# Optimization experiments

Hardware: AMD Instinct MI355X
Metric: run time of the kernel (lower is better)

## Reference

```python
import jax, jax.numpy as jnp
import numpy as np

DIM = 4096
HEADS = 32
HEAD_DIM = 128
FFN_INNER = 4 * DIM  # GEGLU inner
EPS = 1e-6


def _mk(key, shape, scale=0.02):
    return jax.random.normal(key, shape, dtype=jnp.float32) * scale


def setup_inputs() -> dict:
    key = jax.random.key(0)
    ks = jax.random.split(key, 20)
    inp = {
        "video": jax.random.normal(ks[0], (1, 4096, DIM), dtype=jnp.float32),
        "text": jax.random.normal(ks[1], (1, 256, DIM), dtype=jnp.float32),
        # self-attention projections
        "wq": _mk(ks[2], (DIM, DIM)),
        "wk": _mk(ks[3], (DIM, DIM)),
        "wv": _mk(ks[4], (DIM, DIM)),
        "wo": _mk(ks[5], (DIM, DIM)),
        "q_norm_w": jnp.ones((DIM,), jnp.float32),
        "k_norm_w": jnp.ones((DIM,), jnp.float32),
        # cross-attention projections (q from video, k/v from text)
        "cwq": _mk(ks[6], (DIM, DIM)),
        "cwk": _mk(ks[7], (DIM, DIM)),
        "cwv": _mk(ks[8], (DIM, DIM)),
        "cwo": _mk(ks[9], (DIM, DIM)),
        "cq_norm_w": jnp.ones((DIM,), jnp.float32),
        "ck_norm_w": jnp.ones((DIM,), jnp.float32),
        # GEGLU FFN: proj -> (value, gate) -> value * gelu(gate) -> down
        "w_ff_proj": _mk(ks[10], (DIM, 2 * FFN_INNER)),
        "w_ff_down": _mk(ks[11], (FFN_INNER, DIM)),
    }
    return inp


def rmsnorm(x, w, eps=EPS):
    # RMSNorm over full hidden dim in fp32 (matches DistributedRMSNorm global math)
    x32 = x.astype(jnp.float32)
    rms = jax.lax.rsqrt(jnp.mean(x32 * x32, axis=-1, keepdims=True) + eps)
    return (x32 * rms) * w


def split_heads(x):  # [b,s,dim] -> [b,h,s,hd]
    b, s, _ = x.shape
    return x.reshape(b, s, HEADS, HEAD_DIM).transpose(0, 2, 1, 3)


def merge_heads(x):  # [b,h,s,hd] -> [b,s,dim]
    b, h, s, hd = x.shape
    return x.transpose(0, 2, 1, 3).reshape(b, s, h * hd)


def bmm_sdpa(q, k, v):
    # BMM + softmax fallback (explicit score matrix, as on Neuron)
    scale = 1.0 / np.sqrt(HEAD_DIM)
    scores = jnp.einsum("bhqd,bhkd->bhqk", q, k) * scale
    probs = jax.nn.softmax(scores, axis=-1)
    return jnp.einsum("bhqk,bhkd->bhqd", probs, v)


def attention(x_q, x_kv, wq, wk, wv, wo, qn, kn):
    q = rmsnorm(x_q @ wq, qn)
    k = rmsnorm(x_kv @ wk, kn)
    v = x_kv @ wv
    out = bmm_sdpa(split_heads(q), split_heads(k), split_heads(v))
    return merge_heads(out) @ wo


def geglu_ffn(x, w_proj, w_down):
    h = x @ w_proj
    val, gate = jnp.split(h, 2, axis=-1)
    return (val * jax.nn.gelu(gate)) @ w_down


def reference(video, text, wq, wk, wv, wo, q_norm_w, k_norm_w,
              cwq, cwk, cwv, cwo, cq_norm_w, ck_norm_w,
              w_ff_proj, w_ff_down):
    # video self-attention block slice
    h = video + attention(video, video, wq, wk, wv, wo, q_norm_w, k_norm_w)
    # text cross-attention
    h = h + attention(h, text, cwq, cwk, cwv, cwo, cq_norm_w, ck_norm_w)
    # GEGLU feed-forward
    h = h + geglu_ffn(h, w_ff_proj, w_ff_down)
    return h
```

## Files before the change

### kernel.cpp

```cpp
#include <hip/hip_runtime.h>
#include <cstdint>
#include <cstddef>

typedef __bf16 bf16;
typedef __bf16 bf16x8 __attribute__((ext_vector_type(8)));
typedef __bf16 bf16x4 __attribute__((ext_vector_type(4)));
typedef float f32x4 __attribute__((ext_vector_type(4)));

static constexpr int D = 4096;
static constexpr int S = 4096;
static constexpr int T = 256;
static constexpr int H = 32;
static constexpr int F = 16384;

__device__ __forceinline__ void gload16(const void* g, void* l) {
  __builtin_amdgcn_global_load_lds((const __attribute__((address_space(1))) void*)g,
                                   (__attribute__((address_space(3))) void*)l, 16, 0, 0);
}

#define MFMA16(a, b, c) __builtin_amdgcn_mfma_f32_16x16x32_bf16((a), (b), (c), 0, 0, 0)

__global__ __launch_bounds__(256) void k_cvt(const float* __restrict__ in, bf16* __restrict__ out, int n) {
  int i = (blockIdx.x * 256 + threadIdx.x) * 4;
  if (i >= n) return;
  float4 v = *(const float4*)(in + i);
  bf16x4 o = { (bf16)v.x, (bf16)v.y, (bf16)v.z, (bf16)v.w };
  *(bf16x4*)(out + i) = o;
}

__global__ __launch_bounds__(256) void k_tc(const float* __restrict__ in, bf16* __restrict__ out,
                                            int R, int C, int ldin) {
  __shared__ float tile[64][65];
  const int c0 = blockIdx.x * 64, r0 = blockIdx.y * 64;
  const int x = threadIdx.x, y = threadIdx.y;
  #pragma unroll
  for (int i = 0; i < 16; i++) {
    const int yy = y + 4 * i;
    tile[yy][x] = in[(size_t)(r0 + yy) * ldin + c0 + x];
  }
  __syncthreads();
  #pragma unroll
  for (int i = 0; i < 16; i++) {
    const int yy = y + 4 * i;
    out[(size_t)(c0 + yy) * R + r0 + x] = (bf16)tile[x][yy];
  }
}

__global__ __launch_bounds__(256) void k_tb(const bf16* __restrict__ in, bf16* __restrict__ out, int R, int C) {
  __shared__ bf16 tile[32][33];
  int c0 = blockIdx.x * 32, r0 = blockIdx.y * 32;
  int x = threadIdx.x, y = threadIdx.y;
  #pragma unroll
  for (int yy = y; yy < 32; yy += 8)
    tile[yy][x] = in[(size_t)(r0 + yy) * C + c0 + x];
  __syncthreads();
  #pragma unroll
  for (int yy = y; yy < 32; yy += 8)
    out[(size_t)(c0 + yy) * R + r0 + x] = tile[x][yy];
}

__global__ __launch_bounds__(256) void k_rms(const bf16* __restrict__ in, const float* __restrict__ w,
                                             bf16* __restrict__ out) {
  const int row = blockIdx.x, t = threadIdx.x;
  const bf16* x = in + (size_t)row * 4096;
  float xv[16];
  float ss = 0.f;
  #pragma unroll
  for (int i = 0; i < 2; i++) {
    bf16x8 b = *(const bf16x8*)(x + t * 8 + i * 2048);
    #pragma unroll
    for (int j = 0; j < 8; j++) { xv[i * 8 + j] = (float)b[j]; ss += xv[i * 8 + j] * xv[i * 8 + j]; }
  }
  #pragma unroll
  for (int off = 1; off < 64; off <<= 1) ss += __shfl_xor(ss, off, 64);
  __shared__ float red[4];
  if ((t & 63) == 0) red[t >> 6] = ss;
  __syncthreads();
  float rms = rsqrtf((red[0] + red[1] + red[2] + red[3]) * (1.f / 4096.f) + 1e-6f);
  #pragma unroll
  for (int i = 0; i < 2; i++) {
    float4 w0 = *(const float4*)(w + t * 8 + i * 2048);
    float4 w1 = *(const float4*)(w + t * 8 + i * 2048 + 4);
    bf16x8 ov;
    ov[0] = (bf16)(xv[i * 8 + 0] * rms * w0.x); ov[1] = (bf16)(xv[i * 8 + 1] * rms * w0.y);
    ov[2] = (bf16)(xv[i * 8 + 2] * rms * w0.z); ov[3] = (bf16)(xv[i * 8 + 3] * rms * w0.w);
    ov[4] = (bf16)(xv[i * 8 + 4] * rms * w1.x); ov[5] = (bf16)(xv[i * 8 + 5] * rms * w1.y);
    ov[6] = (bf16)(xv[i * 8 + 6] * rms * w1.z); ov[7] = (bf16)(xv[i * 8 + 7] * rms * w1.w);
    *(bf16x8*)(out + (size_t)row * 4096 + t * 8 + i * 2048) = ov;
  }
}

__device__ __forceinline__ void xcd_map(int orig, int XGM, int BYG, int BXG, int& by, int& bx) {
  const int xcd = orig & 7, oidx = orig >> 3;
  by = (xcd % XGM) * BYG + oidx % BYG;
  bx = (xcd / XGM) * BXG + oidx / BYG;
}

template <int MODE>
__global__ __launch_bounds__(512, 2) void k_gemm2(const bf16* __restrict__ A, const bf16* __restrict__ BT,
                                                  float* __restrict__ Cf, bf16* __restrict__ Cb,
                                                  const float* __restrict__ res,
                                                  int M, int N, int K, int XGM, int BYG, int BXG) {
  __shared__ bf16 LA[2][2][256 * 32];
  __shared__ bf16 LB[2][2][256 * 32];
  int by, bx;
  xcd_map(blockIdx.x, XGM, BYG, BXG, by, bx);
  const size_t m0 = (size_t)by * 256, n0 = (size_t)bx * 256;
  const int t = threadIdx.x;
  const int w = t >> 6, lane = t & 63;
  const int wm = w >> 2, wn = w & 3;
  const int g = lane >> 4, r15 = lane & 15;
  const int nt = K >> 6;
  const int sr0 = t >> 2, ss0 = t & 3;
  const int sr1 = (t + 512) >> 2, ss1 = (t + 512) & 3;
  const int sc0 = ((ss0 ^ ((sr0 >> 1) & 3)) << 3);
  const int sc1 = ((ss1 ^ ((sr1 >> 1) & 3)) << 3);
  f32x4 acc[8][4] = {};

  auto stA = [&](int db, int kh, int st) {
    const bf16* src = A + m0 * K + (size_t)st * 64 + kh * 32;
    gload16(src + (size_t)sr0 * K + sc0, &LA[db][kh][t * 8]);
    gload16(src + (size_t)sr1 * K + sc1, &LA[db][kh][(t + 512) * 8]);
  };
  auto stB = [&](int db, int kh, int st) {
    const bf16* src = BT + n0 * K + (size_t)st * 64 + kh * 32;
    gload16(src + (size_t)sr0 * K + sc0, &LB[db][kh][t * 8]);
    gload16(src + (size_t)sr1 * K + sc1, &LB[db][kh][(t + 512) * 8]);
  };

  stA(0, 0, 0); stB(0, 0, 0); stA(0, 1, 0); stB(0, 1, 0);
  stA(1, 0, 1); stB(1, 0, 1); stA(1, 1, 1);
  asm volatile("s_waitcnt vmcnt(10)" ::: "memory");
  __builtin_amdgcn_s_barrier();

  const int arow = wm * 128;

#define GEMM_TILE(DD, TC)                                                                     \
  {                                                                                           \
    const int t1 = ((TC) + 1 < nt) ? (TC) + 1 : nt - 1;                                       \
    const int t2 = ((TC) + 2 < nt) ? (TC) + 2 : nt - 1;                                       \
    bf16x8 af[8], b0, b1;                                                                     \
    stB((DD) ^ 1, 1, t1);                                                                     \
    _Pragma("unroll")                                                                         \
    for (int mf = 0; mf < 8; ++mf) {                                                          \
      const int rr = arow + mf * 16 + r15;                                                    \
      af[mf] = *(const bf16x8*)&LA[DD][0][rr * 32 + ((g ^ ((rr >> 1) & 3)) << 3)];            \
    }                                                                                         \
    {                                                                                         \
      const int rb0 = wn * 64 + r15, rb1 = wn * 64 + 16 + r15;                                \
      b0 = *(const bf16x8*)&LB[DD][0][rb0 * 32 + ((g ^ ((rb0 >> 1) & 3)) << 3)];              \
      b1 = *(const bf16x8*)&LB[DD][0][rb1 * 32 + ((g ^ ((rb1 >> 1) & 3)) << 3)];              \
    }                                                                                         \
    __builtin_amdgcn_s_barrier();                                                             \
    __builtin_amdgcn_s_setprio(1);                                                            \
    _Pragma("unroll")                                                                         \
    for (int mf = 0; mf < 8; ++mf) {                                                          \
      acc[mf][0] = MFMA16(af[mf], b0, acc[mf][0]);                                            \
      acc[mf][1] = MFMA16(af[mf], b1, acc[mf][1]);                                            \
    }                                                                                         \
    __builtin_amdgcn_s_setprio(0);                                                            \
    stA(DD, 0, t2);                                                                           \
    {                                                                                         \
      const int rb0 = wn * 64 + 32 + r15, rb1 = wn * 64 + 48 + r15;                           \
      b0 = *(const bf16x8*)&LB[DD][0][rb0 * 32 + ((g ^ ((rb0 >> 1) & 3)) << 3)];              \
      b1 = *(const bf16x8*)&LB[DD][0][rb1 * 32 + ((g ^ ((rb1 >> 1) & 3)) << 3)];              \
    }                                                                                         \
    asm volatile("s_waitcnt vmcnt(10)" ::: "memory");                                         \
    __builtin_amdgcn_s_barrier();                                                             \
    __builtin_amdgcn_s_setprio(1);                                                            \
    _Pragma("unroll")                                                                         \
    for (int mf = 0; mf < 8; ++mf) {                                                          \
      acc[mf][2] = MFMA16(af[mf], b0, acc[mf][2]);                                            \
      acc[mf][3] = MFMA16(af[mf], b1, acc[mf][3]);                                            \
    }                                                                                         \
    __builtin_amdgcn_s_setprio(0);                                                            \
    stB(DD, 0, t2);                                                                           \
    _Pragma("unroll")                                                                         \
    for (int mf = 0; mf < 8; ++mf) {                                                          \
      const int rr = arow + mf * 16 + r15;                                                    \
      af[mf] = *(const bf16x8*)&LA[DD][1][rr * 32 + ((g ^ ((rr >> 1) & 3)) << 3)];            \
    }                                                                                         \
    {                                                                                         \
      const int rb0 = wn * 64 + r15, rb1 = wn * 64 + 16 + r15;                                \
      b0 = *(const bf16x8*)&LB[DD][1][rb0 * 32 + ((g ^ ((rb0 >> 1) & 3)) << 3)];              \
      b1 = *(const bf16x8*)&LB[DD][1][rb1 * 32 + ((g ^ ((rb1 >> 1) & 3)) << 3)];              \
    }                                                                                         \
    __builtin_amdgcn_s_barrier();                                                             \
    __builtin_amdgcn_s_setprio(1);                                                            \
    _Pragma("unroll")                                                                         \
    for (int mf = 0; mf < 8; ++mf) {                                                          \
      acc[mf][0] = MFMA16(af[mf], b0, acc[mf][0]);                                            \
      acc[mf][1] = MFMA16(af[mf], b1, acc[mf][1]);                                            \
    }                                                                                         \
    __builtin_amdgcn_s_setprio(0);                                                            \
    stA(DD, 1, t2);                                                                           \
    {                                                                                         \
      const int rb0 = wn * 64 + 32 + r15, rb1 = wn * 64 + 48 + r15;                           \
      b0 = *(const bf16x8*)&LB[DD][1][rb0 * 32 + ((g ^ ((rb0 >> 1) & 3)) << 3)];              \
      b1 = *(const bf16x8*)&LB[DD][1][rb1 * 32 + ((g ^ ((rb1 >> 1) & 3)) << 3)];              \
    }                                                                                         \
    asm volatile("s_waitcnt vmcnt(10)" ::: "memory");                                         \
    __builtin_amdgcn_s_barrier();                                                             \
    __builtin_amdgcn_s_setprio(1);                                                            \
    _Pragma("unroll")                                                                         \
    for (int mf = 0; mf < 8; ++mf) {                                                          \
      acc[mf][2] = MFMA16(af[mf], b0, acc[mf][2]);                                            \
      acc[mf][3] = MFMA16(af[mf], b1, acc[mf][3]);                                            \
    }                                                                                         \
    __builtin_amdgcn_s_setprio(0);                                                            \
  }

  for (int tt = 0; tt < nt; tt += 2) {
    GEMM_TILE(0, tt);
    GEMM_TILE(1, tt + 1);
  }
#undef GEMM_TILE

  #pragma unroll
  for (int mf = 0; mf < 8; ++mf)
    #pragma unroll
    for (int nf = 0; nf < 4; ++nf) {
      const size_t col = n0 + wn * 64 + nf * 16 + r15;
      #pragma unroll
      for (int rr = 0; rr < 4; ++rr) {
        const size_t row = m0 + wm * 128 + mf * 16 + g * 4 + rr;
        const size_t idx = row * (size_t)N + col;
        const float v = acc[mf][nf][rr];
        if (MODE == 0) Cf[idx] = v;
        else if (MODE == 1) Cb[idx] = (bf16)v;
        else if (MODE == 2) Cf[idx] = v + res[idx];
        else { const float s = v + res[idx]; Cf[idx] = s; Cb[idx] = (bf16)s; }
      }
    }
}

__global__ __launch_bounds__(512, 2) void k_geglu2(const bf16* __restrict__ A, const bf16* __restrict__ BT,
                                                   bf16* __restrict__ G, int N, int K,
                                                   int XGM, int BYG, int BXG) {
  __shared__ bf16 LA[2][2][256 * 32];
  __shared__ bf16 LBv[2][2][128 * 32];
  __shared__ bf16 LBg[2][2][128 * 32];
  int by, bx;
  xcd_map(blockIdx.x, XGM, BYG, BXG, by, bx);
  const size_t m0 = (size_t)by * 256, n0 = (size_t)bx * 128;
  const int t = threadIdx.x;
  const int w = t >> 6, lane = t & 63;
  const int wm = w >> 2, wn = w & 3;
  const int g = lane >> 4, r15 = lane & 15;
  const int nt = K >> 6;
  const int sr0 = t >> 2, ss0 = t & 3;
  const int sr1 = (t + 512) >> 2, ss1 = (t + 512) & 3;
  const int sc0 = ((ss0 ^ ((sr0 >> 1) & 3)) << 3);
  const int sc1 = ((ss1 ^ ((sr1 >> 1) & 3)) << 3);
  f32x4 av[8][2] = {}, ag[8][2] = {};

  auto stA = [&](int db, int kh, int st) {
    const bf16* src = A + m0 * K + (size_t)st * 64 + kh * 32;
    gload16(src + (size_t)sr0 * K + sc0, &LA[db][kh][t * 8]);
    gload16(src + (size_t)sr1 * K + sc1, &LA[db][kh][(t + 512) * 8]);
  };
  auto stBv = [&](int db, int kh, int st) {
    const bf16* src = BT + n0 * K + (size_t)st * 64 + kh * 32;
    gload16(src + (size_t)sr0 * K + sc0, &LBv[db][kh][t * 8]);
  };
  auto stBg = [&](int db, int kh, int st) {
    const bf16* src = BT + ((size_t)N + n0) * K + (size_t)st * 64 + kh * 32;
    gload16(src + (size_t)sr0 * K + sc0, &LBg[db][kh][t * 8]);
  };

  stA(0, 0, 0); stBv(0, 0, 0); stBg(0, 0, 0); stA(0, 1, 0); stBv(0, 1, 0); stBg(0, 1, 0);
  stA(1, 0, 1); stBv(1, 0, 1); stBg(1, 0, 1); stA(1, 1, 1);
  asm volatile("s_waitcnt vmcnt(10)" ::: "memory");
  __builtin_amdgcn_s_barrier();

  const int arow = wm * 128;

#define GEGLU_TILE(DD, TC)                                                                    \
  {                                                                                           \
    const int t1 = ((TC) + 1 < nt) ? (TC) + 1 : nt - 1;                                       \
    const int t2 = ((TC) + 2 < nt) ? (TC) + 2 : nt - 1;                                       \
    bf16x8 af[8], b0, b1;                                                                     \
    stBv((DD) ^ 1, 1, t1); stBg((DD) ^ 1, 1, t1);                                             \
    _Pragma("unroll")                                                                         \
    for (int mf = 0; mf < 8; ++mf) {                                                          \
      const int rr = arow + mf * 16 + r15;                                                    \
      af[mf] = *(const bf16x8*)&LA[DD][0][rr * 32 + ((g ^ ((rr >> 1) & 3)) << 3)];            \
    }                                                                                         \
    {                                                                                         \
      const int rb0 = wn * 32 + r15, rb1 = wn * 32 + 16 + r15;                                \
      b0 = *(const bf16x8*)&LBv[DD][0][rb0 * 32 + ((g ^ ((rb0 >> 1) & 3)) << 3)];             \
      b1 = *(const bf16x8*)&LBv[DD][0][rb1 * 32 + ((g ^ ((rb1 >> 1) & 3)) << 3)];             \
    }                                                                                         \
    __builtin_amdgcn_s_barrier();                                                             \
    __builtin_amdgcn_s_setprio(1);                                                            \
    _Pragma("unroll")                                                                         \
    for (int mf = 0; mf < 8; ++mf) {                                                          \
      av[mf][0] = MFMA16(af[mf], b0, av[mf][0]);                                              \
      av[mf][1] = MFMA16(af[mf], b1, av[mf][1]);                                              \
    }                                                                                         \
    __builtin_amdgcn_s_setprio(0);                                                            \
    stA(DD, 0, t2);                                                                           \
    {                                                                                         \
      const int rb0 = wn * 32 + r15, rb1 = wn * 32 + 16 + r15;                                \
      b0 = *(const bf16x8*)&LBg[DD][0][rb0 * 32 + ((g ^ ((rb0 >> 1) & 3)) << 3)];             \
      b1 = *(const bf16x8*)&LBg[DD][0][rb1 * 32 + ((g ^ ((rb1 >> 1) & 3)) << 3)];             \
    }                                                                                         \
    asm volatile("s_waitcnt vmcnt(10)" ::: "memory");                                         \
    __builtin_amdgcn_s_barrier();                                                             \
    __builtin_amdgcn_s_setprio(1);                                                            \
    _Pragma("unroll")                                                                         \
    for (int mf = 0; mf < 8; ++mf) {                                                          \
      ag[mf][0] = MFMA16(af[mf], b0, ag[mf][0]);                                              \
      ag[mf][1] = MFMA16(af[mf], b1, ag[mf][1]);                                              \
    }                                                                                         \
    __builtin_amdgcn_s_setprio(0);                                                            \
    stBv(DD, 0, t2); stBg(DD, 0, t2);                                                         \
    _Pragma("unroll")                                                                         \
    for (int mf = 0; mf < 8; ++mf) {                                                          \
      const int rr = arow + mf * 16 + r15;                                                    \
      af[mf] = *(const bf16x8*)&LA[DD][1][rr * 32 + ((g ^ ((rr >> 1) & 3)) << 3)];            \
    }                                                                                         \
    {                                                                                         \
      const int rb0 = wn * 32 + r15, rb1 = wn * 32 + 16 + r15;                                \
      b0 = *(const bf16x8*)&LBv[DD][1][rb0 * 32 + ((g ^ ((rb0 >> 1) & 3)) << 3)];             \
      b1 = *(const bf16x8*)&LBv[DD][1][rb1 * 32 + ((g ^ ((rb1 >> 1) & 3)) << 3)];             \
    }                                                                                         \
    __builtin_amdgcn_s_barrier();                                                             \
    __builtin_amdgcn_s_setprio(1);                                                            \
    _Pragma("unroll")                                                                         \
    for (int mf = 0; mf < 8; ++mf) {                                                          \
      av[mf][0] = MFMA16(af[mf], b0, av[mf][0]);                                              \
      av[mf][1] = MFMA16(af[mf], b1, av[mf][1]);                                              \
    }                                                                                         \
    __builtin_amdgcn_s_setprio(0);                                                            \
    stA(DD, 1, t2);                                                                           \
    {                                                                                         \
      const int rb0 = wn * 32 + r15, rb1 = wn * 32 + 16 + r15;                                \
      b0 = *(const bf16x8*)&LBg[DD][1][rb0 * 32 + ((g ^ ((rb0 >> 1) & 3)) << 3)];             \
      b1 = *(const bf16x8*)&LBg[DD][1][rb1 * 32 + ((g ^ ((rb1 >> 1) & 3)) << 3)];             \
    }                                                                                         \
    asm volatile("s_waitcnt vmcnt(10)" ::: "memory");                                         \
    __builtin_amdgcn_s_barrier();                                                             \
    __builtin_amdgcn_s_setprio(1);                                                            \
    _Pragma("unroll")                                                                         \
    for (int mf = 0; mf < 8; ++mf) {                                                          \
      ag[mf][0] = MFMA16(af[mf], b0, ag[mf][0]);                                              \
      ag[mf][1] = MFMA16(af[mf], b1, ag[mf][1]);                                              \
    }                                                                                         \
    __builtin_amdgcn_s_setprio(0);                                                            \
  }

  for (int tt = 0; tt < nt; tt += 2) {
    GEGLU_TILE(0, tt);
    GEGLU_TILE(1, tt + 1);
  }
#undef GEGLU_TILE

  #pragma unroll
  for (int mf = 0; mf < 8; ++mf)
    #pragma unroll
    for (int nf = 0; nf < 2; ++nf) {
      const size_t col = n0 + wn * 32 + nf * 16 + r15;
      #pragma unroll
      for (int rr = 0; rr < 4; ++rr) {
        const size_t row = m0 + wm * 128 + mf * 16 + g * 4 + rr;
        const float val = av[mf][nf][rr], gt = ag[mf][nf][rr];
        const float z = 1.595769122f * gt + 0.0713548162f * gt * gt * gt;
        const float gel = gt / (1.f + __expf(-z));
        G[row * (size_t)N + col] = (bf16)(val * gel);
      }
    }
}

template <int MODE>
__global__ __launch_bounds__(256) void k_gemm128(const bf16* __restrict__ A, const bf16* __restrict__ BT,
                                                 float* __restrict__ Cf, bf16* __restrict__ Cb,
                                                 int M, int N, int K) {
  __shared__ bf16 As[128 * 32];
  __shared__ bf16 Bs[128 * 32];
  const int t = threadIdx.x;
// ... 16 lines not shown
    bf16x8 af[4], bfr[4];
    #pragma unroll
    for (int mi = 0; mi < 4; mi++) {
      int row = wr * 64 + mi * 16 + r15;
      af[mi] = *(const bf16x8*)&As[row * 32 + ((g ^ (row & 3)) << 3)];
    }
    #pragma unroll
    for (int ni = 0; ni < 4; ni++) {
      int row = wc * 64 + ni * 16 + r15;
      bfr[ni] = *(const bf16x8*)&Bs[row * 32 + ((g ^ (row & 3)) << 3)];
    }
    #pragma unroll
    for (int mi = 0; mi < 4; mi++)
      #pragma unroll
      for (int ni = 0; ni < 4; ni++)
        acc[mi][ni] = MFMA16(af[mi], bfr[ni], acc[mi][ni]);
  }
  #pragma unroll
  for (int mi = 0; mi < 4; mi++)
    #pragma unroll
    for (int ni = 0; ni < 4; ni++) {
      size_t col = n0 + wc * 64 + ni * 16 + r15;
      #pragma unroll
      for (int rr = 0; rr < 4; rr++) {
        size_t row = m0 + wr * 64 + mi * 16 + g * 4 + rr;
        size_t idx = row * (size_t)N + col;
        float v = acc[mi][ni][rr];
        if (MODE == 0) Cf[idx] = v;
        else Cb[idx] = (bf16)v;
      }
    }
}

__global__ __launch_bounds__(256) void k_attn(const bf16* __restrict__ Q, const bf16* __restrict__ Kb,
                                              const bf16* __restrict__ VT, bf16* __restrict__ O,
                                              int Skv) {
  __shared__ bf16 Kt[64 * 128];
  __shared__ bf16 Vt[128 * 64];
  __shared__ bf16 Pt[4][16 * 64];
  const int h = blockIdx.y;
  const int t = threadIdx.x, w = t >> 6, lane = t & 63;
  const int g = lane >> 4, r15 = lane & 15;
  const int q0 = blockIdx.x * 64 + w * 16;
  bf16x8 qf[4];
  #pragma unroll
  for (int c = 0; c < 4; c++)
    qf[c] = *(const bf16x8*)(Q + (size_t)(q0 + r15) * D + h * 128 + c * 32 + g * 8);
  f32x4 o[8] = {};
  float m_[4] = { -1e30f, -1e30f, -1e30f, -1e30f };
  float l_[4] = { 0.f, 0.f, 0.f, 0.f };
  const float scale = 0.08838834764831845f;
  for (int kt = 0; kt < Skv; kt += 64) {
    __syncthreads();
    #pragma unroll
    for (int cc = 0; cc < 4; cc++) {
      int c = t + cc * 256;
      int kr = c >> 4, ks = c & 15;
      gload16(Kb + (size_t)(kt + kr) * D + h * 128 + ((ks ^ (kr & 15)) << 3), &Kt[c * 8]);
      int vr = c >> 3, vs = c & 7;
      gload16(VT + (size_t)(h * 128 + vr) * Skv + kt + ((vs ^ (vr & 7)) << 3), &Vt[c * 8]);
    }
    __syncthreads();
    f32x4 s[4] = {};
    __builtin_amdgcn_s_setprio(1);
    #pragma unroll
    for (int c = 0; c < 4; c++) {
      #pragma unroll
      for (int j = 0; j < 4; j++) {
        const int row = j * 16 + r15;
        bf16x8 kf = *(const bf16x8*)&Kt[row * 128 + (((4 * c + g) ^ (row & 15)) << 3)];
        s[j] = MFMA16(qf[c], kf, s[j]);
      }
    }
    __builtin_amdgcn_s_setprio(0);
    float al[4];
    #pragma unroll
    for (int rr = 0; rr < 4; rr++) {
      float v0 = s[0][rr] * scale, v1 = s[1][rr] * scale;
      float v2 = s[2][rr] * scale, v3 = s[3][rr] * scale;
      float mx = fmaxf(fmaxf(v0, v1), fmaxf(v2, v3));
      #pragma unroll
      for (int off = 1; off < 16; off <<= 1) mx = fmaxf(mx, __shfl_xor(mx, off, 16));
      float mn = fmaxf(m_[rr], mx);
      al[rr] = __expf(m_[rr] - mn);
      float p0 = __expf(v0 - mn), p1 = __expf(v1 - mn);
      float p2 = __expf(v2 - mn), p3 = __expf(v3 - mn);
      float sm = p0 + p1 + p2 + p3;
      #pragma unroll
      for (int off = 1; off < 16; off <<= 1) sm += __shfl_xor(sm, off, 16);
      l_[rr] = l_[rr] * al[rr] + sm;
      m_[rr] = mn;
      const int prow = g * 4 + rr;
      const int sbase = prow * 64, sx = prow & 7, e = r15 & 7, hi = r15 >> 3;
      Pt[w][sbase + (((0 + hi) ^ sx) << 3) + e] = (bf16)p0;
      Pt[w][sbase + (((2 + hi) ^ sx) << 3) + e] = (bf16)p1;
      Pt[w][sbase + (((4 + hi) ^ sx) << 3) + e] = (bf16)p2;
      Pt[w][sbase + (((6 + hi) ^ sx) << 3) + e] = (bf16)p3;
    }
    #pragma unroll
    for (int d = 0; d < 8; d++)
      #pragma unroll
      for (int rr = 0; rr < 4; rr++) o[d][rr] *= al[rr];
    bf16x8 pa[2];
    #pragma unroll
    for (int kk = 0; kk < 2; kk++)
      pa[kk] = *(const bf16x8*)&Pt[w][r15 * 64 + (((kk * 4 + g) ^ (r15 & 7)) << 3)];
    __builtin_amdgcn_s_setprio(1);
    #pragma unroll
    for (int d = 0; d < 8; d++) {
      const int vrow = d * 16 + r15;
      #pragma unroll
      for (int kk = 0; kk < 2; kk++) {
        bf16x8 vbf = *(const bf16x8*)&Vt[vrow * 64 + (((kk * 4 + g) ^ (vrow & 7)) << 3)];
        o[d] = MFMA16(pa[kk], vbf, o[d]);
      }
    }
    __builtin_amdgcn_s_setprio(0);
  }
  #pragma unroll
  for (int rr = 0; rr < 4; rr++) {
    float inv = 1.f / l_[rr];
    #pragma unroll
    for (int d = 0; d < 8; d++)
      O[(size_t)(q0 + g * 4 + rr) * D + h * 128 + d * 16 + r15] = (bf16)(o[d][rr] * inv);
  }
}

extern "C" void kernel_launch(void* const* d_in, const int* in_sizes, int n_in,
                              void* d_out, int out_size, void* d_ws, size_t ws_size,
                              hipStream_t stream) {
  (void)in_sizes; (void)n_in; (void)out_size; (void)ws_size;
  const float* video = (const float*)d_in[0];
  const float* text  = (const float*)d_in[1];
  const float* wq    = (const float*)d_in[2];
  const float* wk    = (const float*)d_in[3];
  const float* wv    = (const float*)d_in[4];
  const float* wo    = (const float*)d_in[5];
  const float* qnw   = (const float*)d_in[6];
  const float* knw   = (const float*)d_in[7];
  const float* cwq   = (const float*)d_in[8];
  const float* cwk   = (const float*)d_in[9];
  const float* cwv   = (const float*)d_in[10];
  const float* cwo   = (const float*)d_in[11];
  const float* cqnw  = (const float*)d_in[12];
  const float* cknw  = (const float*)d_in[13];
  const float* ffp   = (const float*)d_in[14];
  const float* ffd   = (const float*)d_in[15];
  float* out = (float*)d_out;

  char* slab = (char*)d_ws;
  const size_t MB = 1024 * 1024;
  bf16*  wbuf  = (bf16*)slab;
  bf16*  vb    = (bf16*)(slab + 64 * MB);
  bf16*  vt    = (bf16*)(slab + 96 * MB);
  bf16*  preb  = (bf16*)(slab + 128 * MB);
  bf16*  Hval  = (bf16*)(slab + 268 * MB);
  char* p = slab + 402 * MB;
  auto take = [&](size_t bytes) { char* r = p; p += (bytes + 255) & ~(size_t)255; return r; };
  bf16* xb   = (bf16*)take((size_t)S * D * 2);
  bf16* qb   = (bf16*)take((size_t)S * D * 2);
  bf16* kb   = (bf16*)take((size_t)S * D * 2);
  bf16* ab   = (bf16*)take((size_t)S * D * 2);
  float* h1  = (float*)take((size_t)S * D * 4);
  bf16* tbuf = (bf16*)take((size_t)T * D * 2);
  bf16* ckb  = (bf16*)take((size_t)T * D * 2);
  bf16* cvb  = (bf16*)take((size_t)T * D * 2);
  bf16* cvt_ = (bf16*)take((size_t)T * D * 2);
  float* h2  = out;

  dim3 b256(256), b512(512), btc(64, 4), btb(32, 8);
  const int GRID_DD = 256, GRID_GG = 2048;

  k_cvt<<<(S * D) / 1024, b256, 0, stream>>>(video, xb, S * D);
  k_tc<<<dim3(D / 64, D / 64), btc, 0, stream>>>(wq, wbuf, D, D, D);
  k_gemm2<1><<<GRID_DD, b512, 0, stream>>>(xb, wbuf, nullptr, preb, nullptr, S, D, D, 2, 8, 4);
  k_rms<<<S, b256, 0, stream>>>(preb, qnw, qb);
  k_tc<<<dim3(D / 64, D / 64), btc, 0, stream>>>(wk, wbuf, D, D, D);
  k_gemm2<1><<<GRID_DD, b512, 0, stream>>>(xb, wbuf, nullptr, preb, nullptr, S, D, D, 2, 8, 4);
  k_rms<<<S, b256, 0, stream>>>(preb, knw, kb);
  k_tc<<<dim3(D / 64, D / 64), btc, 0, stream>>>(wv, wbuf, D, D, D);
  k_gemm2<1><<<GRID_DD, b512, 0, stream>>>(xb, wbuf, nullptr, vb, nullptr, S, D, D, 2, 8, 4);
  k_tb<<<dim3(D / 32, S / 32), btb, 0, stream>>>(vb, vt, S, D);
  k_attn<<<dim3(S / 64, H), b256, 0, stream>>>(qb, kb, vt, ab, S);
  k_tc<<<dim3(D / 64, D / 64), btc, 0, stream>>>(wo, wbuf, D, D, D);
  k_gemm2<3><<<GRID_DD, b512, 0, stream>>>(ab, wbuf, h1, xb, video, S, D, D, 2, 8, 4);

  k_tc<<<dim3(D / 64, D / 64), btc, 0, stream>>>(cwq, wbuf, D, D, D);
  k_gemm2<1><<<GRID_DD, b512, 0, stream>>>(xb, wbuf, nullptr, preb, nullptr, S, D, D, 2, 8, 4);
  k_rms<<<S, b256, 0, stream>>>(preb, cqnw, qb);
  k_cvt<<<(T * D) / 1024, b256, 0, stream>>>(text, tbuf, T * D);
  k_tc<<<dim3(D / 64, D / 64), btc, 0, stream>>>(cwk, wbuf, D, D, D);
  k_gemm128<1><<<dim3(D / 128, T / 128), b256, 0, stream>>>(tbuf, wbuf, nullptr, preb, T, D, D);
  k_rms<<<T, b256, 0, stream>>>(preb, cknw, ckb);
  k_tc<<<dim3(D / 64, D / 64), btc, 0, stream>>>(cwv, wbuf, D, D, D);
  k_gemm128<1><<<dim3(D / 128, T / 128), b256, 0, stream>>>(tbuf, wbuf, nullptr, cvb, T, D, D);
  k_tb<<<dim3(D / 32, T / 32), btb, 0, stream>>>(cvb, cvt_, T, D);
  k_attn<<<dim3(S / 64, H), b256, 0, stream>>>(qb, ckb, cvt_, ab, T);
  k_tc<<<dim3(D / 64, D / 64), btc, 0, stream>>>(cwo, wbuf, D, D, D);
  k_gemm2<3><<<GRID_DD, b512, 0, stream>>>(ab, wbuf, h2, xb, h1, S, D, D, 2, 8, 4);

  k_tc<<<dim3((2 * F) / 64, D / 64), btc, 0, stream>>>(ffp, wbuf, D, 2 * F, 2 * F);
  k_geglu2<<<GRID_GG, b512, 0, stream>>>(xb, wbuf, Hval, F, D, 2, 8, 32);
  k_tc<<<dim3(D / 64, F / 64), btc, 0, stream>>>(ffd, wbuf, F, D, D);
  k_gemm2<2><<<GRID_DD, b512, 0, stream>>>(Hval, wbuf, out, nullptr, h2, S, D, F, 2, 8, 4);
}
```

Before: 3.646 ms.

## Restructure GEMM and GEGLU main loops into two phases per K-half

Both bf16 GEMM main loops (plain and GEGLU dual-B) change from four barrier-separated MFMA phases per tile to two. Each phase now loads all B fragments at once and issues 32 MFMAs, and the global-to-LDS prefetch is regrouped so the A and B halves are issued together, with the vmcnt waits adjusted to match. The aim is to halve barrier and waitcnt stalls and give longer uninterrupted MFMA bursts. The cost is more live B registers, and the changed prefetch timing and wait counts could expose load latency or a race if the counts are wrong.

```diff
diff --git a/kernel.cpp b/kernel.cpp
--- a/kernel.cpp
+++ b/kernel.cpp
@@ -129,8 +129,8 @@
   };
 
   stA(0, 0, 0); stB(0, 0, 0); stA(0, 1, 0); stB(0, 1, 0);
-  stA(1, 0, 1); stB(1, 0, 1); stA(1, 1, 1);
-  asm volatile("s_waitcnt vmcnt(10)" ::: "memory");
+  stA(1, 0, 1); stB(1, 0, 1);
+  asm volatile("s_waitcnt vmcnt(8)" ::: "memory");
   __builtin_amdgcn_s_barrier();
 
   const int arow = wm * 128;
@@ -139,8 +139,9 @@
   {                                                                                           \
     const int t1 = ((TC) + 1 < nt) ? (TC) + 1 : nt - 1;                                       \
     const int t2 = ((TC) + 2 < nt) ? (TC) + 2 : nt - 1;                                       \
-    bf16x8 af[8], b0, b1;                                                                     \
-    stB((DD) ^ 1, 1, t1);                                                                     \
+    bf16x8 af[8], b0, b1, b2, b3;                                                             \
+                                                           \
+    stA((DD) ^ 1, 1, t1); stB((DD) ^ 1, 1, t1);                                               \
     _Pragma("unroll")                                                                         \
     for (int mf = 0; mf < 8; ++mf) {                                                          \
       const int rr = arow + mf * 16 + r15;                                                    \
@@ -148,64 +149,47 @@
     }                                                                                         \
     {                                                                                         \
       const int rb0 = wn * 64 + r15, rb1 = wn * 64 + 16 + r15;                                \
+      const int rb2 = wn * 64 + 32 + r15, rb3 = wn * 64 + 48 + r15;                           \
       b0 = *(const bf16x8*)&LB[DD][0][rb0 * 32 + ((g ^ ((rb0 >> 1) & 3)) << 3)];              \
       b1 = *(const bf16x8*)&LB[DD][0][rb1 * 32 + ((g ^ ((rb1 >> 1) & 3)) << 3)];              \
-    }                                                                                         \
+      b2 = *(const bf16x8*)&LB[DD][0][rb2 * 32 + ((g ^ ((rb2 >> 1) & 3)) << 3)];              \
+      b3 = *(const bf16x8*)&LB[DD][0][rb3 * 32 + ((g ^ ((rb3 >> 1) & 3)) << 3)];              \
+    }                                                                                         \
+    asm volatile("s_waitcnt vmcnt(12)" ::: "memory");                                         \
     __builtin_amdgcn_s_barrier();                                                             \
     __builtin_amdgcn_s_setprio(1);                                                            \
     _Pragma("unroll")                                                                         \
     for (int mf = 0; mf < 8; ++mf) {                                                          \
       acc[mf][0] = MFMA16(af[mf], b0, acc[mf][0]);                                            \
       acc[mf][1] = MFMA16(af[mf], b1, acc[mf][1]);                                            \
+      acc[mf][2] = MFMA16(af[mf], b2, acc[mf][2]);                                            \
+      acc[mf][3] = MFMA16(af[mf], b3, acc[mf][3]);                                            \
     }                                                                                         \
     __builtin_amdgcn_s_setprio(0);                                                            \
-    stA(DD, 0, t2);                                                                           \
+                                                                           \
+    stA(DD, 0, t2); stB(DD, 0, t2);                                                           \
+    _Pragma("unroll")                                                                         \
+    for (int mf = 0; mf < 8; ++mf) {                                                          \
+      const int rr = arow + mf * 16 + r15;                                                    \
+      af[mf] = *(const bf16x8*)&LA[DD][1][rr * 32 + ((g ^ ((rr >> 1) & 3)) << 3)];            \
+    }                                                                                         \
     {                                                                                         \
-      const int rb0 = wn * 64 + 32 + r15, rb1 = wn * 64 + 48 + r15;                           \
-      b0 = *(const bf16x8*)&LB[DD][0][rb0 * 32 + ((g ^ ((rb0 >> 1) & 3)) << 3)];              \
-      b1 = *(const bf16x8*)&LB[DD][0][rb1 * 32 + ((g ^ ((rb1 >> 1) & 3)) << 3)];              \
-    }                                                                                         \
-    asm volatile("s_waitcnt vmcnt(10)" ::: "memory");                                         \
+      const int rb0 = wn * 64 + r15, rb1 = wn * 64 + 16 + r15;                                \
+      const int rb2 = wn * 64 + 32 + r15, rb3 = wn * 64 + 48 + r15;                           \
+      b0 = *(const bf16x8*)&LB[DD][1][rb0 * 32 + ((g ^ ((rb0 >> 1) & 3)) << 3)];              \
+      b1 = *(const bf16x8*)&LB[DD][1][rb1 * 32 + ((g ^ ((rb1 >> 1) & 3)) << 3)];              \
+      b2 = *(const bf16x8*)&LB[DD][1][rb2 * 32 + ((g ^ ((rb2 >> 1) & 3)) << 3)];              \
+      b3 = *(const bf16x8*)&LB[DD][1][rb3 * 32 + ((g ^ ((rb3 >> 1) & 3)) << 3)];              \
+    }                                                                                         \
+    asm volatile("s_waitcnt vmcnt(12)" ::: "memory");                                         \
     __builtin_amdgcn_s_barrier();                                                             \
     __builtin_amdgcn_s_setprio(1);                                                            \
     _Pragma("unroll")                                                                         \
     for (int mf = 0; mf < 8; ++mf) {                                                          \
-      acc[mf][2] = MFMA16(af[mf], b0, acc[mf][2]);                                            \
-      acc[mf][3] = MFMA16(af[mf], b1, acc[mf][3]);                                            \
-    }                                                                                         \
-    __builtin_amdgcn_s_setprio(0);                                                            \
-    stB(DD, 0, t2);                                                                           \
-    _Pragma("unroll")                                                                         \
-    for (int mf = 0; mf < 8; ++mf) {                                                          \
-      const int rr = arow + mf * 16 + r15;                                                    \
-      af[mf] = *(const bf16x8*)&LA[DD][1][rr * 32 + ((g ^ ((rr >> 1) & 3)) << 3)];            \
-    }                                                                                         \
-    {                                                                                         \
-      const int rb0 = wn * 64 + r15, rb1 = wn * 64 + 16 + r15;                                \
-      b0 = *(const bf16x8*)&LB[DD][1][rb0 * 32 + ((g ^ ((rb0 >> 1) & 3)) << 3)];              \
-      b1 = *(const bf16x8*)&LB[DD][1][rb1 * 32 + ((g ^ ((rb1 >> 1) & 3)) << 3)];              \
-    }                                                                                         \
-    __builtin_amdgcn_s_barrier();                                                             \
-    __builtin_amdgcn_s_setprio(1);                                                            \
-    _Pragma("unroll")                                                                         \
-    for (int mf = 0; mf < 8; ++mf) {                                                          \
       acc[mf][0] = MFMA16(af[mf], b0, acc[mf][0]);                                            \
       acc[mf][1] = MFMA16(af[mf], b1, acc[mf][1]);                                            \
-    }                                                                                         \
-    __builtin_amdgcn_s_setprio(0);                                                            \
-    stA(DD, 1, t2);                                                                           \
-    {                                                                                         \
-      const int rb0 = wn * 64 + 32 + r15, rb1 = wn * 64 + 48 + r15;                           \
-      b0 = *(const bf16x8*)&LB[DD][1][rb0 * 32 + ((g ^ ((rb0 >> 1) & 3)) << 3)];              \
-      b1 = *(const bf16x8*)&LB[DD][1][rb1 * 32 + ((g ^ ((rb1 >> 1) & 3)) << 3)];              \
-    }                                                                                         \
-    asm volatile("s_waitcnt vmcnt(10)" ::: "memory");                                         \
-    __builtin_amdgcn_s_barrier();                                                             \
-    __builtin_amdgcn_s_setprio(1);                                                            \
-    _Pragma("unroll")                                                                         \
-    for (int mf = 0; mf < 8; ++mf) {                                                          \
-      acc[mf][2] = MFMA16(af[mf], b0, acc[mf][2]);                                            \
-      acc[mf][3] = MFMA16(af[mf], b1, acc[mf][3]);                                            \
+      acc[mf][2] = MFMA16(af[mf], b2, acc[mf][2]);                                            \
+      acc[mf][3] = MFMA16(af[mf], b3, acc[mf][3]);                                            \
     }                                                                                         \
     __builtin_amdgcn_s_setprio(0);                                                            \
   }
@@ -269,8 +253,8 @@
   };
 
   stA(0, 0, 0); stBv(0, 0, 0); stBg(0, 0, 0); stA(0, 1, 0); stBv(0, 1, 0); stBg(0, 1, 0);
-  stA(1, 0, 1); stBv(1, 0, 1); stBg(1, 0, 1); stA(1, 1, 1);
-  asm volatile("s_waitcnt vmcnt(10)" ::: "memory");
+  stA(1, 0, 1); stBv(1, 0, 1); stBg(1, 0, 1);
+  asm volatile("s_waitcnt vmcnt(8)" ::: "memory");
   __builtin_amdgcn_s_barrier();
 
   const int arow = wm * 128;
@@ -279,8 +263,9 @@
   {                                                                                           \
     const int t1 = ((TC) + 1 < nt) ? (TC) + 1 : nt - 1;                                       \
     const int t2 = ((TC) + 2 < nt) ? (TC) + 2 : nt - 1;                                       \
-    bf16x8 af[8], b0, b1;                                                                     \
-    stBv((DD) ^ 1, 1, t1); stBg((DD) ^ 1, 1, t1);                                             \
+    bf16x8 af[8], b0, b1, b2, b3;                                                             \
+                                                              \
+    stA((DD) ^ 1, 1, t1); stBv((DD) ^ 1, 1, t1); stBg((DD) ^ 1, 1, t1);                       \
     _Pragma("unroll")                                                                         \
     for (int mf = 0; mf < 8; ++mf) {                                                          \
       const int rr = arow + mf * 16 + r15;                                                    \
@@ -290,31 +275,22 @@
       const int rb0 = wn * 32 + r15, rb1 = wn * 32 + 16 + r15;                                \
       b0 = *(const bf16x8*)&LBv[DD][0][rb0 * 32 + ((g ^ ((rb0 >> 1) & 3)) << 3)];             \
       b1 = *(const bf16x8*)&LBv[DD][0][rb1 * 32 + ((g ^ ((rb1 >> 1) & 3)) << 3)];             \
-    }                                                                                         \
+      b2 = *(const bf16x8*)&LBg[DD][0][rb0 * 32 + ((g ^ ((rb0 >> 1) & 3)) << 3)];             \
+      b3 = *(const bf16x8*)&LBg[DD][0][rb1 * 32 + ((g ^ ((rb1 >> 1) & 3)) << 3)];             \
+    }                                                                                         \
+    asm volatile("s_waitcnt vmcnt(12)" ::: "memory");                                         \
     __builtin_amdgcn_s_barrier();                                                             \
     __builtin_amdgcn_s_setprio(1);                                                            \
     _Pragma("unroll")                                                                         \
     for (int mf = 0; mf < 8; ++mf) {                                                          \
       av[mf][0] = MFMA16(af[mf], b0, av[mf][0]);                                              \
       av[mf][1] = MFMA16(af[mf], b1, av[mf][1]);                                              \
+      ag[mf][0] = MFMA16(af[mf], b2, ag[mf][0]);                                              \
+      ag[mf][1] = MFMA16(af[mf], b3, ag[mf][1]);                                              \
     }                                                                                         \
     __builtin_amdgcn_s_setprio(0);                                                            \
-    stA(DD, 0, t2);                                                                           \
-    {                                                                                         \
-      const int rb0 = wn * 32 + r15, rb1 = wn * 32 + 16 + r15;                                \
-      b0 = *(const bf16x8*)&LBg[DD][0][rb0 * 32 + ((g ^ ((rb0 >> 1) & 3)) << 3)];             \
-      b1 = *(const bf16x8*)&LBg[DD][0][rb1 * 32 + ((g ^ ((rb1 >> 1) & 3)) << 3)];             \
-    }                                                                                         \
-    asm volatile("s_waitcnt vmcnt(10)" ::: "memory");                                         \
-    __builtin_amdgcn_s_barrier();                                                             \
-    __builtin_amdgcn_s_setprio(1);                                                            \
-    _Pragma("unroll")                                                                         \
-    for (int mf = 0; mf < 8; ++mf) {                                                          \
-      ag[mf][0] = MFMA16(af[mf], b0, ag[mf][0]);                                              \
-      ag[mf][1] = MFMA16(af[mf], b1, ag[mf][1]);                                              \
-    }                                                                                         \
-    __builtin_amdgcn_s_setprio(0);                                                            \
-    stBv(DD, 0, t2); stBg(DD, 0, t2);                                                         \
+                                                                           \
+    stA(DD, 0, t2); stBv(DD, 0, t2); stBg(DD, 0, t2);                                         \
     _Pragma("unroll")                                                                         \
     for (int mf = 0; mf < 8; ++mf) {                                                          \
       const int rr = arow + mf * 16 + r15;                                                    \
@@ -324,28 +300,18 @@
       const int rb0 = wn * 32 + r15, rb1 = wn * 32 + 16 + r15;                                \
       b0 = *(const bf16x8*)&LBv[DD][1][rb0 * 32 + ((g ^ ((rb0 >> 1) & 3)) << 3)];             \
       b1 = *(const bf16x8*)&LBv[DD][1][rb1 * 32 + ((g ^ ((rb1 >> 1) & 3)) << 3)];             \
-    }                                                                                         \
+      b2 = *(const bf16x8*)&LBg[DD][1][rb0 * 32 + ((g ^ ((rb0 >> 1) & 3)) << 3)];             \
+      b3 = *(const bf16x8*)&LBg[DD][1][rb1 * 32 + ((g ^ ((rb1 >> 1) & 3)) << 3)];             \
+    }                                                                                         \
+    asm volatile("s_waitcnt vmcnt(12)" ::: "memory");                                         \
     __builtin_amdgcn_s_barrier();                                                             \
     __builtin_amdgcn_s_setprio(1);                                                            \
     _Pragma("unroll")                                                                         \
     for (int mf = 0; mf < 8; ++mf) {                                                          \
       av[mf][0] = MFMA16(af[mf], b0, av[mf][0]);                                              \
       av[mf][1] = MFMA16(af[mf], b1, av[mf][1]);                                              \
-    }                                                                                         \
-    __builtin_amdgcn_s_setprio(0);                                                            \
-    stA(DD, 1, t2);                                                                           \
-    {                                                                                         \
-      const int rb0 = wn * 32 + r15, rb1 = wn * 32 + 16 + r15;                                \
-      b0 = *(const bf16x8*)&LBg[DD][1][rb0 * 32 + ((g ^ ((rb0 >> 1) & 3)) << 3)];             \
-      b1 = *(const bf16x8*)&LBg[DD][1][rb1 * 32 + ((g ^ ((rb1 >> 1) & 3)) << 3)];             \
-    }                                                                                         \
-    asm volatile("s_waitcnt vmcnt(10)" ::: "memory");                                         \
-    __builtin_amdgcn_s_barrier();                                                             \
-    __builtin_amdgcn_s_setprio(1);                                                            \
-    _Pragma("unroll")                                                                         \
-    for (int mf = 0; mf < 8; ++mf) {                                                          \
-      ag[mf][0] = MFMA16(af[mf], b0, ag[mf][0]);                                              \
-      ag[mf][1] = MFMA16(af[mf], b1, ag[mf][1]);                                              \
+      ag[mf][0] = MFMA16(af[mf], b2, ag[mf][0]);                                              \
+      ag[mf][1] = MFMA16(af[mf], b3, ag[mf][1]);                                              \
     }                                                                                         \
     __builtin_amdgcn_s_setprio(0);                                                            \
   }
```

After: 3.728 ms. 2.2% more time.

## Double attention query tile per block and reuse K smem for P

Applied to the files above, without the earlier changes.

The attention kernel now uses 512 threads covering 128 query rows per block, so each K/V tile loaded into shared memory serves twice as many queries. The per-wave P buffer is aliased onto the K tile region after an extra barrier, which keeps LDS use unchanged. The online softmax rescale of the accumulator is skipped when no row maximum in the wave grows. The cost is one more __syncthreads per KV tile and half as many blocks in the grid.

```diff
diff --git a/kernel.cpp b/kernel.cpp
--- a/kernel.cpp
+++ b/kernel.cpp
@@ -428,16 +428,16 @@
     }
 }
 
-__global__ __launch_bounds__(256) void k_attn(const bf16* __restrict__ Q, const bf16* __restrict__ Kb,
+__global__ __launch_bounds__(512) void k_attn(const bf16* __restrict__ Q, const bf16* __restrict__ Kb,
                                               const bf16* __restrict__ VT, bf16* __restrict__ O,
                                               int Skv) {
   __shared__ bf16 Kt[64 * 128];
   __shared__ bf16 Vt[128 * 64];
-  __shared__ bf16 Pt[4][16 * 64];
   const int h = blockIdx.y;
   const int t = threadIdx.x, w = t >> 6, lane = t & 63;
   const int g = lane >> 4, r15 = lane & 15;
-  const int q0 = blockIdx.x * 64 + w * 16;
+  const int q0 = blockIdx.x * 128 + w * 16;
+  bf16* PtW = &Kt[w * 1024];
   bf16x8 qf[4];
   #pragma unroll
   for (int c = 0; c < 4; c++)
@@ -449,8 +449,8 @@
   for (int kt = 0; kt < Skv; kt += 64) {
     __syncthreads();
     #pragma unroll
-    for (int cc = 0; cc < 4; cc++) {
-      int c = t + cc * 256;
+    for (int cc = 0; cc < 2; cc++) {
+      int c = t + cc * 512;
       int kr = c >> 4, ks = c & 15;
       gload16(Kb + (size_t)(kt + kr) * D + h * 128 + ((ks ^ (kr & 15)) << 3), &Kt[c * 8]);
       int vr = c >> 3, vs = c & 7;
@@ -469,38 +469,53 @@
       }
     }
     __builtin_amdgcn_s_setprio(0);
-    float al[4];
+    __syncthreads();
+    float sv[4][4], mxs[4];
+    bool grow = false;
     #pragma unroll
     for (int rr = 0; rr < 4; rr++) {
       float v0 = s[0][rr] * scale, v1 = s[1][rr] * scale;
       float v2 = s[2][rr] * scale, v3 = s[3][rr] * scale;
+      sv[rr][0] = v0; sv[rr][1] = v1; sv[rr][2] = v2; sv[rr][3] = v3;
       float mx = fmaxf(fmaxf(v0, v1), fmaxf(v2, v3));
       #pragma unroll
       for (int off = 1; off < 16; off <<= 1) mx = fmaxf(mx, __shfl_xor(mx, off, 16));
-      float mn = fmaxf(m_[rr], mx);
-      al[rr] = __expf(m_[rr] - mn);
-      float p0 = __expf(v0 - mn), p1 = __expf(v1 - mn);
-      float p2 = __expf(v2 - mn), p3 = __expf(v3 - mn);
+      mxs[rr] = mx;
+      grow = grow || (mx > m_[rr]);
+    }
+    if (__any(grow ? 1 : 0)) {
+      float al[4];
+      #pragma unroll
+      for (int rr = 0; rr < 4; rr++) {
+        float mn = fmaxf(m_[rr], mxs[rr]);
+        al[rr] = __expf(m_[rr] - mn);
+        l_[rr] *= al[rr];
+        m_[rr] = mn;
+      }
+      #pragma unroll
+      for (int d = 0; d < 8; d++)
+        #pragma unroll
+        for (int rr = 0; rr < 4; rr++) o[d][rr] *= al[rr];
+    }
+    #pragma unroll
+    for (int rr = 0; rr < 4; rr++) {
+      float p0 = __expf(sv[rr][0] - m_[rr]), p1 = __expf(sv[rr][1] - m_[rr]);
+      float p2 = __expf(sv[rr][2] - m_[rr]), p3 = __expf(sv[rr][3] - m_[rr]);
       float sm = p0 + p1 + p2 + p3;
       #pragma unroll
       for (int off = 1; off < 16; off <<= 1) sm += __shfl_xor(sm, off, 16);
-      l_[rr] = l_[rr] * al[rr] + sm;
-      m_[rr] = mn;
+      l_[rr] += sm;
       const int prow = g * 4 + rr;
       const int sbase = prow * 64, sx = prow & 7, e = r15 & 7, hi = r15 >> 3;
-      Pt[w][sbase + (((0 + hi) ^ sx) << 3) + e] = (bf16)p0;
-      Pt[w][sbase + (((2 + hi) ^ sx) << 3) + e] = (bf16)p1;
-      Pt[w][sbase + (((4 + hi) ^ sx) << 3) + e] = (bf16)p2;
-      Pt[w][sbase + (((6 + hi) ^ sx) << 3) + e] = (bf16)p3;
-    }
-    #pragma unroll
-    for (int d = 0; d < 8; d++)
-      #pragma unroll
-      for (int rr = 0; rr < 4; rr++) o[d][rr] *= al[rr];
+      PtW[sbase + (((0 + hi) ^ sx) << 3) + e] = (bf16)p0;
+      PtW[sbase + (((2 + hi) ^ sx) << 3) + e] = (bf16)p1;
+      PtW[sbase + (((4 + hi) ^ sx) << 3) + e] = (bf16)p2;
+      PtW[sbase + (((6 + hi) ^ sx) << 3) + e] = (bf16)p3;
+    }
     bf16x8 pa[2];
     #pragma unroll
     for (int kk = 0; kk < 2; kk++)
-      pa[kk] = *(const bf16x8*)&Pt[w][r15 * 64 + (((kk * 4 + g) ^ (r15 & 7)) << 3)];
+      pa[kk] = *(const bf16x8*)&PtW[r15 * 64 + (((kk * 4 + g) ^ (r15 & 7)) << 3)];
     __builtin_amdgcn_s_setprio(1);
     #pragma unroll
     for (int d = 0; d < 8; d++) {
@@ -577,7 +592,7 @@
   k_tc<<<dim3(D / 64, D / 64), btc, 0, stream>>>(wv, wbuf, D, D, D);
   k_gemm2<1><<<GRID_DD, b512, 0, stream>>>(xb, wbuf, nullptr, vb, nullptr, S, D, D, 2, 8, 4);
   k_tb<<<dim3(D / 32, S / 32), btb, 0, stream>>>(vb, vt, S, D);
-  k_attn<<<dim3(S / 64, H), b256, 0, stream>>>(qb, kb, vt, ab, S);
+  k_attn<<<dim3(S / 128, H), b512, 0, stream>>>(qb, kb, vt, ab, S);
   k_tc<<<dim3(D / 64, D / 64), btc, 0, stream>>>(wo, wbuf, D, D, D);
   k_gemm2<3><<<GRID_DD, b512, 0, stream>>>(ab, wbuf, h1, xb, video, S, D, D, 2, 8, 4);
 
@@ -591,7 +606,7 @@
   k_tc<<<dim3(D / 64, D / 64), btc, 0, stream>>>(cwv, wbuf, D, D, D);
   k_gemm128<1><<<dim3(D / 128, T / 128), b256, 0, stream>>>(tbuf, wbuf, nullptr, cvb, T, D, D);
   k_tb<<<dim3(D / 32, T / 32), btb, 0, stream>>>(cvb, cvt_, T, D);
-  k_attn<<<dim3(S / 64, H), b256, 0, stream>>>(qb, ckb, cvt_, ab, T);
+  k_attn<<<dim3(S / 128, H), b512, 0, stream>>>(qb, ckb, cvt_, ab, T);
   k_tc<<<dim3(D / 64, D / 64), btc, 0, stream>>>(cwo, wbuf, D, D, D);
   k_gemm2<3><<<GRID_DD, b512, 0, stream>>>(ab, wbuf, h2, xb, h1, S, D, D, 2, 8, 4);
 
```

Measured after the change: 3.715 ms. About the same (+1.9%).

## Fuse self-attention QKV projections into one GEMM and skip unneeded softmax rescales

Applied to the files above, without the earlier changes.

Transposes wq, wk and wv into one contiguous weight buffer and runs a single GEMM with N=3D, writing a strided QKV output. RMSNorm and the V transpose then read from that output using a leading-dimension argument, which removes two GEMM launches and their tail effects. The softmax scale is folded into the Q RMSNorm. The attention kernel now rescales the accumulator only when some row maximum grows, which skips the exp and multiply work on most key tiles. This adds a wave-wide vote branch and puts the scaled Q in bf16, which slightly changes rounding.

```diff
diff --git a/kernel.cpp b/kernel.cpp
--- a/kernel.cpp
+++ b/kernel.cpp
@@ -46,13 +46,14 @@
   }
 }
 
-__global__ __launch_bounds__(256) void k_tb(const bf16* __restrict__ in, bf16* __restrict__ out, int R, int C) {
+__global__ __launch_bounds__(256) void k_tb(const bf16* __restrict__ in, bf16* __restrict__ out,
+                                            int R, int C, int ldin) {
   __shared__ bf16 tile[32][33];
   int c0 = blockIdx.x * 32, r0 = blockIdx.y * 32;
   int x = threadIdx.x, y = threadIdx.y;
   #pragma unroll
   for (int yy = y; yy < 32; yy += 8)
-    tile[yy][x] = in[(size_t)(r0 + yy) * C + c0 + x];
+    tile[yy][x] = in[(size_t)(r0 + yy) * ldin + c0 + x];
   __syncthreads();
   #pragma unroll
   for (int yy = y; yy < 32; yy += 8)
@@ -60,9 +61,9 @@
 }
 
 __global__ __launch_bounds__(256) void k_rms(const bf16* __restrict__ in, const float* __restrict__ w,
-                                             bf16* __restrict__ out) {
+                                             bf16* __restrict__ out, int ldin, float sc) {
   const int row = blockIdx.x, t = threadIdx.x;
-  const bf16* x = in + (size_t)row * 4096;
+  const bf16* x = in + (size_t)row * ldin;
   float xv[16];
   float ss = 0.f;
   #pragma unroll
@@ -76,7 +77,7 @@
   __shared__ float red[4];
   if ((t & 63) == 0) red[t >> 6] = ss;
   __syncthreads();
-  float rms = rsqrtf((red[0] + red[1] + red[2] + red[3]) * (1.f / 4096.f) + 1e-6f);
+  float rms = rsqrtf((red[0] + red[1] + red[2] + red[3]) * (1.f / 4096.f) + 1e-6f) * sc;
   #pragma unroll
   for (int i = 0; i < 2; i++) {
     float4 w0 = *(const float4*)(w + t * 8 + i * 2048);
@@ -194,7 +195,7 @@
     }                                                                                         \
     __builtin_amdgcn_s_setprio(0);                                                            \
     stA(DD, 1, t2);                                                                           \
-    {                                                                                         \
+    {                                                                                           \
       const int rb0 = wn * 64 + 32 + r15, rb1 = wn * 64 + 48 + r15;                           \
       b0 = *(const bf16x8*)&LB[DD][1][rb0 * 32 + ((g ^ ((rb0 >> 1) & 3)) << 3)];              \
       b1 = *(const bf16x8*)&LB[DD][1][rb1 * 32 + ((g ^ ((rb1 >> 1) & 3)) << 3)];              \
@@ -445,7 +446,6 @@
   f32x4 o[8] = {};
   float m_[4] = { -1e30f, -1e30f, -1e30f, -1e30f };
   float l_[4] = { 0.f, 0.f, 0.f, 0.f };
-  const float scale = 0.08838834764831845f;
   for (int kt = 0; kt < Skv; kt += 64) {
     __syncthreads();
     #pragma unroll
@@ -469,23 +469,39 @@
       }
     }
     __builtin_amdgcn_s_setprio(0);
-    float al[4];
+    float sv[4][4], mxs[4];
+    bool grow = false;
     #pragma unroll
     for (int rr = 0; rr < 4; rr++) {
-      float v0 = s[0][rr] * scale, v1 = s[1][rr] * scale;
-      float v2 = s[2][rr] * scale, v3 = s[3][rr] * scale;
-      float mx = fmaxf(fmaxf(v0, v1), fmaxf(v2, v3));
+      sv[rr][0] = s[0][rr]; sv[rr][1] = s[1][rr]; sv[rr][2] = s[2][rr]; sv[rr][3] = s[3][rr];
+      float mx = fmaxf(fmaxf(sv[rr][0], sv[rr][1]), fmaxf(sv[rr][2], sv[rr][3]));
       #pragma unroll
       for (int off = 1; off < 16; off <<= 1) mx = fmaxf(mx, __shfl_xor(mx, off, 16));
-      float mn = fmaxf(m_[rr], mx);
-      al[rr] = __expf(m_[rr] - mn);
-      float p0 = __expf(v0 - mn), p1 = __expf(v1 - mn);
-      float p2 = __expf(v2 - mn), p3 = __expf(v3 - mn);
+      mxs[rr] = mx;
+      grow = grow || (mx > m_[rr]);
+    }
+    if (__any(grow ? 1 : 0)) {
+      float al[4];
+      #pragma unroll
+      for (int rr = 0; rr < 4; rr++) {
+        float mn = fmaxf(m_[rr], mxs[rr]);
+        al[rr] = __expf(m_[rr] - mn);
+        l_[rr] *= al[rr];
+        m_[rr] = mn;
+      }
+      #pragma unroll
+      for (int d = 0; d < 8; d++)
+        #pragma unroll
+        for (int rr = 0; rr < 4; rr++) o[d][rr] *= al[rr];
+    }
+    #pragma unroll
+    for (int rr = 0; rr < 4; rr++) {
+      float p0 = __expf(sv[rr][0] - m_[rr]), p1 = __expf(sv[rr][1] - m_[rr]);
+      float p2 = __expf(sv[rr][2] - m_[rr]), p3 = __expf(sv[rr][3] - m_[rr]);
       float sm = p0 + p1 + p2 + p3;
       #pragma unroll
       for (int off = 1; off < 16; off <<= 1) sm += __shfl_xor(sm, off, 16);
-      l_[rr] = l_[rr] * al[rr] + sm;
-      m_[rr] = mn;
+      l_[rr] += sm;
       const int prow = g * 4 + rr;
       const int sbase = prow * 64, sx = prow & 7, e = r15 & 7, hi = r15 >> 3;
       Pt[w][sbase + (((0 + hi) ^ sx) << 3) + e] = (bf16)p0;
@@ -493,10 +509,6 @@
       Pt[w][sbase + (((4 + hi) ^ sx) << 3) + e] = (bf16)p2;
       Pt[w][sbase + (((6 + hi) ^ sx) << 3) + e] = (bf16)p3;
     }
-    #pragma unroll
-    for (int d = 0; d < 8; d++)
-      #pragma unroll
-      for (int rr = 0; rr < 4; rr++) o[d][rr] *= al[rr];
     bf16x8 pa[2];
     #pragma unroll
     for (int kk = 0; kk < 2; kk++)
@@ -543,14 +555,14 @@
   const float* ffp   = (const float*)d_in[14];
   const float* ffd   = (const float*)d_in[15];
   float* out = (float*)d_out;
+  const float SCQ = 0.08838834764831845f;
 
   char* slab = (char*)d_ws;
   const size_t MB = 1024 * 1024;
-  bf16*  wbuf  = (bf16*)slab;
-  bf16*  vb    = (bf16*)(slab + 64 * MB);
-  bf16*  vt    = (bf16*)(slab + 96 * MB);
-  bf16*  preb  = (bf16*)(slab + 128 * MB);
-  bf16*  Hval  = (bf16*)(slab + 268 * MB);
+  bf16*  wbuf   = (bf16*)slab;
+  bf16*  vt     = (bf16*)(slab + 96 * MB);
+  bf16*  preqkv = (bf16*)(slab + 128 * MB);
+  bf16*  Hval   = (bf16*)(slab + 268 * MB);
   char* p = slab + 402 * MB;
   auto take = [&](size_t bytes) { char* r = p; p += (bytes + 255) & ~(size_t)255; return r; };
   bf16* xb   = (bf16*)take((size_t)S * D * 2);
@@ -565,32 +577,30 @@
   float* h2  = out;
 
   dim3 b256(256), b512(512), btc(64, 4), btb(32, 8);
-  const int GRID_DD = 256, GRID_GG = 2048;
+  const int GRID_DD = 256, GRID_GG = 2048, GRID_QKV = 768;
 
   k_cvt<<<(S * D) / 1024, b256, 0, stream>>>(video, xb, S * D);
   k_tc<<<dim3(D / 64, D / 64), btc, 0, stream>>>(wq, wbuf, D, D, D);
-  k_gemm2<1><<<GRID_DD, b512, 0, stream>>>(xb, wbuf, nullptr, preb, nullptr, S, D, D, 2, 8, 4);
-  k_rms<<<S, b256, 0, stream>>>(preb, qnw, qb);
-  k_tc<<<dim3(D / 64, D / 64), btc, 0, stream>>>(wk, wbuf, D, D, D);
-  k_gemm2<1><<<GRID_DD, b512, 0, stream>>>(xb, wbuf, nullptr, preb, nullptr, S, D, D, 2, 8, 4);
-  k_rms<<<S, b256, 0, stream>>>(preb, knw, kb);
-  k_tc<<<dim3(D / 64, D / 64), btc, 0, stream>>>(wv, wbuf, D, D, D);
-  k_gemm2<1><<<GRID_DD, b512, 0, stream>>>(xb, wbuf, nullptr, vb, nullptr, S, D, D, 2, 8, 4);
-  k_tb<<<dim3(D / 32, S / 32), btb, 0, stream>>>(vb, vt, S, D);
+  k_tc<<<dim3(D / 64, D / 64), btc, 0, stream>>>(wk, wbuf + (size_t)D * D, D, D, D);
+  k_tc<<<dim3(D / 64, D / 64), btc, 0, stream>>>(wv, wbuf + 2 * (size_t)D * D, D, D, D);
+  k_gemm2<1><<<GRID_QKV, b512, 0, stream>>>(xb, wbuf, nullptr, preqkv, nullptr, S, 3 * D, D, 2, 8, 12);
+  k_rms<<<S, b256, 0, stream>>>(preqkv, qnw, qb, 3 * D, SCQ);
+  k_rms<<<S, b256, 0, stream>>>(preqkv + D, knw, kb, 3 * D, 1.f);
+  k_tb<<<dim3(D / 32, S / 32), btb, 0, stream>>>(preqkv + 2 * D, vt, S, D, 3 * D);
   k_attn<<<dim3(S / 64, H), b256, 0, stream>>>(qb, kb, vt, ab, S);
   k_tc<<<dim3(D / 64, D / 64), btc, 0, stream>>>(wo, wbuf, D, D, D);
   k_gemm2<3><<<GRID_DD, b512, 0, stream>>>(ab, wbuf, h1, xb, video, S, D, D, 2, 8, 4);
 
   k_tc<<<dim3(D / 64, D / 64), btc, 0, stream>>>(cwq, wbuf, D, D, D);
-  k_gemm2<1><<<GRID_DD, b512, 0, stream>>>(xb, wbuf, nullptr, preb, nullptr, S, D, D, 2, 8, 4);
-  k_rms<<<S, b256, 0, stream>>>(preb, cqnw, qb);
+  k_gemm2<1><<<GRID_DD, b512, 0, stream>>>(xb, wbuf, nullptr, preqkv, nullptr, S, D, D, 2, 8, 4);
+  k_rms<<<S, b256, 0, stream>>>(preqkv, cqnw, qb, D, SCQ);
   k_cvt<<<(T * D) / 1024, b256, 0, stream>>>(text, tbuf, T * D);
   k_tc<<<dim3(D / 64, D / 64), btc, 0, stream>>>(cwk, wbuf, D, D, D);
-  k_gemm128<1><<<dim3(D / 128, T / 128), b256, 0, stream>>>(tbuf, wbuf, nullptr, preb, T, D, D);
-  k_rms<<<T, b256, 0, stream>>>(preb, cknw, ckb);
+  k_gemm128<1><<<dim3(D / 128, T / 128), b256, 0, stream>>>(tbuf, wbuf, nullptr, preqkv, T, D, D);
+  k_rms<<<T, b256, 0, stream>>>(preqkv, cknw, ckb, D, 1.f);
   k_tc<<<dim3(D / 64, D / 64), btc, 0, stream>>>(cwv, wbuf, D, D, D);
   k_gemm128<1><<<dim3(D / 128, T / 128), b256, 0, stream>>>(tbuf, wbuf, nullptr, cvb, T, D, D);
-  k_tb<<<dim3(D / 32, T / 32), btb, 0, stream>>>(cvb, cvt_, T, D);
+  k_tb<<<dim3(D / 32, T / 32), btb, 0, stream>>>(cvb, cvt_, T, D, D);
   k_attn<<<dim3(S / 64, H), b256, 0, stream>>>(qb, ckb, cvt_, ab, T);
   k_tc<<<dim3(D / 64, D / 64), btc, 0, stream>>>(cwo, wbuf, D, D, D);
   k_gemm2<3><<<GRID_DD, b512, 0, stream>>>(ab, wbuf, h2, xb, h1, S, D, D, 2, 8, 4);
```

New measurement: 3.651 ms. No clear change (+0.1%).
